# Performance work log

Measured on AMD Instinct MI355X. Metric: run time of the kernel, lower is better.

## Reference

```python
import jax, jax.numpy as jnp
import numpy as np

B, T, D = 8, 1, 4096          # batch, fresh tokens (single-token decode), d_model
H, HD, KV = 32, 128, 512      # n_heads, head_dim, mla_kv_lrank
PAST = 8191                   # cached compressed-KV length
SCALE = HD ** -0.5


def setup_inputs() -> dict:
    key = jax.random.key(0)
    ks = jax.random.split(key, 6)
    return {
        "x": jax.random.normal(ks[0], (B, T, D), dtype=jnp.float32),
        "past_c": jax.random.normal(ks[1], (B, PAST, KV), dtype=jnp.float32),
        # absorbed q*k_up projection: [H, D, KV]
        "absorbed_qk": jax.random.normal(ks[2], (H, D, KV), dtype=jnp.float32) * 0.02,
        # _compress_kv: Linear(D -> KV)
        "w_compress": jax.random.normal(ks[3], (D, KV), dtype=jnp.float32) * 0.02,
        # v_up: Linear(KV -> H*HD)
        "w_v": jax.random.normal(ks[4], (KV, H * HD), dtype=jnp.float32) * 0.02,
        # out_proj: Linear(H*HD -> D)
        "w_o": jax.random.normal(ks[5], (H * HD, D), dtype=jnp.float32) * 0.02,
    }


def reference(x, past_c, absorbed_qk, w_compress, w_v, w_o):
    b, t, d = x.shape
    # compress fresh tokens and extend the compressed KV cache
    c = x @ w_compress                                 # [B, T, KV]
    c_full = jnp.concatenate([past_c, c], axis=1)      # [B, total, KV]
    total = c_full.shape[1]

    # absorbed query projection: Q_abs = x @ absorbed_qk per head
    q_abs = jnp.einsum('btd,hdk->bhtk', x, absorbed_qk)        # [B, H, T, KV]
    # attention scores directly against compressed cache
    scores = jnp.einsum('bhtk,bsk->bhts', q_abs, c_full) * SCALE  # [B, H, T, total]

    # causal mask: query t (absolute pos total-T+t) sees kv pos p iff p <= total-T+t
    q_pos = jnp.arange(t)[:, None] + (total - t)       # [T, 1]
    kv_pos = jnp.arange(total)[None, :]                # [1, total]
    causal = q_pos >= kv_pos                           # [T, total]
    scores = jnp.where(causal[None, None], scores, -jnp.inf)
    attn = jax.nn.softmax(scores, axis=-1)             # [B, H, T, total]

    # up-project V from compressed cache
    v = (c_full @ w_v).reshape(b, total, H, HD)        # [B, total, H, HD]
    out = jnp.einsum('bhts,bshd->bthd', attn, v).reshape(b, t, H * HD)
    return out @ w_o                                   # [B, T, D]
```

## Files before the change

### kernel.cpp

```cpp
#include <hip/hip_runtime.h>
#include <stdint.h>

#define B_ 8
#define D_ 4096
#define H_ 32
#define HD_ 128
#define KV_ 512
#define PAST_ 8191
#define SCALE_ 0.08838834764831845f

#define OFF_QP   0u
#define OFF_CP   2097152u
#define OFF_QABS 2162688u
#define OFF_CNEW 2293760u
#define OFF_ML   2297856u
#define OFF_CTXP 2330624u
#define OFF_CTX2 10719232u

typedef float f32x4 __attribute__((ext_vector_type(4)));
typedef float f32x2 __attribute__((ext_vector_type(2)));
typedef short s16x8 __attribute__((ext_vector_type(8)));
typedef short s16x4 __attribute__((ext_vector_type(4)));

__device__ __forceinline__ unsigned short f2bf(float f) {
    unsigned u = __float_as_uint(f);
    u = (u + 0x7FFFu + ((u >> 16) & 1u)) >> 16;
    return (unsigned short)u;
}
__device__ __forceinline__ float bf2f(unsigned short s) {
    return __uint_as_float(((unsigned)s) << 16);
}

__global__ __launch_bounds__(128) void k_qabs(const float* __restrict__ x,
                                              const float* __restrict__ aqk,
                                              const float* __restrict__ wc,
                                              float* __restrict__ ws) {
    const int h = blockIdx.x;
    const int dc = blockIdx.y;
    const int t = threadIdx.x;
    alignas(16) __shared__ float x_lds[B_][256];
    for (int i = t; i < 512; i += 128) {
        const int b = i >> 6, g = i & 63;
        *(f32x4*)&x_lds[b][g * 4] = *(const f32x4*)(x + (size_t)b * D_ + dc * 256 + g * 4);
    }
    __syncthreads();
    const float* A = (h < H_) ? (aqk + (size_t)h * D_ * KV_) : wc;
    A += ((size_t)dc * 256) * KV_ + t * 4;

    f32x4 acc[B_];
#pragma unroll
    for (int b = 0; b < B_; ++b) acc[b] = (f32x4){0.f, 0.f, 0.f, 0.f};

#pragma unroll 2
    for (int dd = 0; dd < 256; dd += 4) {
        const f32x4 a0 = *(const f32x4*)(A + (size_t)(dd + 0) * KV_);
        const f32x4 a1 = *(const f32x4*)(A + (size_t)(dd + 1) * KV_);
        const f32x4 a2 = *(const f32x4*)(A + (size_t)(dd + 2) * KV_);
        const f32x4 a3 = *(const f32x4*)(A + (size_t)(dd + 3) * KV_);
#pragma unroll
        for (int b = 0; b < B_; ++b) {
            const f32x4 xq = *(const f32x4*)&x_lds[b][dd];
            acc[b] += xq.x * a0 + xq.y * a1 + xq.z * a2 + xq.w * a3;
        }
    }
#pragma unroll
    for (int b = 0; b < B_; ++b) {
        float* dst = (h < H_)
            ? (ws + OFF_QP + (size_t)dc * 131072u + (size_t)(b * H_ + h) * KV_ + t * 4)
            : (ws + OFF_CP + (size_t)dc * 4096u + (size_t)b * KV_ + t * 4);
        *(f32x4*)dst = acc[b];
    }
}

__global__ __launch_bounds__(256) void k_qred(float* __restrict__ ws) {
    const int bx = blockIdx.x;
    const int t = threadIdx.x;
    if (bx < 256) {
        const int b = bx >> 5, h = bx & 31;
        const size_t row = (size_t)(b * H_ + h) * KV_;
        f32x2 s = {0.f, 0.f};
#pragma unroll
        for (int p = 0; p < 16; ++p) {
            const f32x2 v = *(const f32x2*)(ws + OFF_QP + (size_t)p * 131072u + row + 2 * t);
            s[0] += v[0]; s[1] += v[1];
        }
        *(f32x2*)(ws + OFF_QABS + row + 2 * t) = s;
    } else {
        const int b = bx - 256;
        f32x2 s = {0.f, 0.f};
#pragma unroll
        for (int p = 0; p < 16; ++p) {
            const f32x2 v = *(const f32x2*)(ws + OFF_CP + (size_t)p * 4096u + (size_t)b * KV_ + 2 * t);
            s[0] += v[0]; s[1] += v[1];
        }
        *(f32x2*)(ws + OFF_CNEW + (size_t)b * KV_ + 2 * t) = s;
    }
}

__global__ __launch_bounds__(256, 2) void k_attn(const float* __restrict__ past_c,
                                                 float* __restrict__ ws) {
    const int bx = blockIdx.x;
    const int b = bx >> 6, sc = bx & 63;
    const int t = threadIdx.x;
    const int w = t >> 6, lane = t & 63, quad = lane >> 4, ln = lane & 15;
    const int ni = w & 1, kh = w >> 1;

    alignas(16) __shared__ unsigned short ch[16 * 520];
    alignas(16) __shared__ unsigned short cl[16 * 520];
    alignas(16) __shared__ unsigned short cT[512 * 20];
    alignas(16) __shared__ float Sp[2 * 16 * 33];
    alignas(16) __shared__ unsigned short P[32 * 20];
    __shared__ float alpha[32];

    s16x8 qh[8], ql[8];
    {
        const float* qp = ws + OFF_QABS + (size_t)(b * H_ + ni * 16 + ln) * KV_ + kh * 256 + quad * 8;
#pragma unroll
        for (int st = 0; st < 8; ++st) {
            const f32x4 v0 = *(const f32x4*)(qp + st * 32);
            const f32x4 v1 = *(const f32x4*)(qp + st * 32 + 4);
#pragma unroll
            for (int i = 0; i < 8; ++i) {
                const float xv = ((i < 4) ? v0[i] : v1[i - 4]) * SCALE_;
                const unsigned short hi = f2bf(xv);
                qh[st][i] = (short)hi;
                ql[st][i] = (short)f2bf(xv - bf2f(hi));
            }
        }
    }

    f32x4 cacc[16];
#pragma unroll
    for (int i = 0; i < 16; ++i) cacc[i] = (f32x4){0.f, 0.f, 0.f, 0.f};
    float m_run = -1e30f, l_run = 0.f;

    for (int sub = 0; sub < 8; ++sub) {
        const int s0 = sc * 128 + sub * 16;
        {
            const int r = t >> 4, m = t & 15;
            const int sg = s0 + r;
            const float* src = (sg == PAST_) ? (ws + OFF_CNEW + (size_t)b * KV_)
                                             : (past_c + ((size_t)b * PAST_ + sg) * KV_);
#pragma unroll
            for (int i = 0; i < 8; ++i) {
                const int k = m * 4 + i * 64;
                const f32x4 v = *(const f32x4*)(src + k);
                s16x4 hi4, lo4;
#pragma unroll
                for (int e = 0; e < 4; ++e) {
                    const unsigned short hh = f2bf(v[e]);
                    hi4[e] = (short)hh;
                    lo4[e] = (short)f2bf(v[e] - bf2f(hh));
                    const int kk = k + e;
                    cT[kk * 20 + (r ^ ((((kk) >> 4) & 3) << 2))] = hh;
                }
                *(s16x4*)&ch[r * 520 + k] = hi4;
                *(s16x4*)&cl[r * 520 + k] = lo4;
            }
        }
        __syncthreads();
        {
            f32x4 sacc = {0.f, 0.f, 0.f, 0.f};
#pragma unroll
            for (int st = 0; st < 8; ++st) {
                const int ko = kh * 256 + st * 32 + quad * 8;
                const s16x8 ah = *(const s16x8*)&ch[ln * 520 + ko];
                const s16x8 al = *(const s16x8*)&cl[ln * 520 + ko];
                sacc = __builtin_amdgcn_mfma_f32_16x16x32_bf16(ah, qh[st], sacc, 0, 0, 0);
                sacc = __builtin_amdgcn_mfma_f32_16x16x32_bf16(ah, ql[st], sacc, 0, 0, 0);
                sacc = __builtin_amdgcn_mfma_f32_16x16x32_bf16(al, qh[st], sacc, 0, 0, 0);
            }
#pragma unroll
            for (int r = 0; r < 4; ++r)
                Sp[kh * 528 + (quad * 4 + r) * 33 + ni * 16 + ln] = sacc[r];
        }
        __syncthreads();
        if (t < 32) {
            const int h = t;
            float sv[16];
            float msub = -1e30f;
#pragma unroll
            for (int s = 0; s < 16; ++s) {
                sv[s] = Sp[s * 33 + h] + Sp[528 + s * 33 + h];
                msub = fmaxf(msub, sv[s]);
            }
            const float m_new = fmaxf(m_run, msub);
            const float al_ = __expf(m_run - m_new);
            float lsum = 0.f;
#pragma unroll
            for (int s = 0; s < 16; s += 2) {
                const float p0 = __expf(sv[s] - m_new);
                const float p1 = __expf(sv[s + 1] - m_new);
                lsum += p0 + p1;
                const unsigned pk = (unsigned)f2bf(p0) | ((unsigned)f2bf(p1) << 16);
                *(unsigned*)&P[h * 20 + s] = pk;
            }
            l_run = l_run * al_ + lsum;
            m_run = m_new;
            alpha[h] = al_;
        }
        __syncthreads();
        {
            const float av = alpha[ni * 16 + ln];
            const s16x4 bp = *(const s16x4*)&P[(ni * 16 + ln) * 20 + quad * 4];
#pragma unroll
            for (int ti = 0; ti < 16; ++ti) {
                const int krow = (kh * 16 + ti) * 16 + ln;
                const int sg2 = (quad ^ ((krow >> 4) & 3)) << 2;
                const s16x4 ac = *(const s16x4*)&cT[krow * 20 + sg2];
                f32x4 cc = cacc[ti];
                cc[0] *= av; cc[1] *= av; cc[2] *= av; cc[3] *= av;
                cacc[ti] = __builtin_amdgcn_mfma_f32_16x16x16bf16_1k(ac, bp, cc, 0, 0, 0);
            }
        }
        __syncthreads();
    }
    {
        float* cp = ws + OFF_CTXP + ((size_t)(b * 64 + sc) * H_ + (ni * 16 + ln)) * KV_;
#pragma unroll
        for (int ti = 0; ti < 16; ++ti) {
            const int k0 = (kh * 16 + ti) * 16 + quad * 4;
            *(f32x4*)(cp + k0) = cacc[ti];
        }
    }
    if (t < 32) {
        float* mp = ws + OFF_ML + (size_t)(b * 64 + sc) * 64;
        mp[t] = m_run;
        mp[32 + t] = l_run;
    }
}

__global__ __launch_bounds__(256) void k_cv(const float* __restrict__ wv,
                                            float* __restrict__ ws) {
    const int b = blockIdx.x >> 5, h = blockIdx.x & 31;
    const int t = threadIdx.x;
    __shared__ float ml[64], ll[64], wgt[64];
    alignas(16) __shared__ float cx[512];
    alignas(16) __shared__ float red[8][128];
    if (t < 64) {
        const float* mp = ws + OFF_ML + (size_t)(b * 64 + t) * 64;
        ml[t] = mp[h];
        ll[t] = mp[32 + h];
    }
    __syncthreads();
    float M = -1e30f;
    for (int s = 0; s < 64; ++s) M = fmaxf(M, ml[s]);
    if (t < 64) wgt[t] = __expf(ml[t] - M);
    __syncthreads();
    float L = 0.f;
    for (int s = 0; s < 64; ++s) L += ll[s] * wgt[s];
    const float invL = 1.f / L;
    f32x2 acc = {0.f, 0.f};
    for (int s = 0; s < 64; ++s) {
        const float f = wgt[s];
        const f32x2 v = *(const f32x2*)(ws + OFF_CTXP + ((size_t)(b * 64 + s) * H_ + h) * KV_ + 2 * t);
        acc[0] += f * v[0];
        acc[1] += f * v[1];
    }
    *(f32x2*)&cx[2 * t] = (f32x2){acc[0] * invL, acc[1] * invL};
    __syncthreads();
    const int r = t >> 5, c = (t & 31) * 4;
    f32x4 a4 = {0.f, 0.f, 0.f, 0.f};
    for (int kb = 0; kb < 64; ++kb) {
        const int k = kb * 8 + r;
        const f32x4 w4 = *(const f32x4*)(wv + (size_t)k * (H_ * HD_) + h * HD_ + c);
        a4 += cx[k] * w4;
    }
    *(f32x4*)&red[r][c] = a4;
    __syncthreads();
    if (t < 128) {
        float s = 0.f;
#pragma unroll
        for (int rr = 0; rr < 8; ++rr) s += red[rr][t];
        ws[OFF_CTX2 + (size_t)b * D_ + h * HD_ + t] = s;
    }
}

__global__ __launch_bounds__(256) void k_out(const float* __restrict__ wo,
                                             const float* __restrict__ ws,
                                             float* __restrict__ out) {
    const int dc = blockIdx.x, jc = blockIdx.y;
    const int t = threadIdx.x;
    alignas(16) __shared__ float c2[B_][256];
#pragma unroll
    for (int i = 0; i < 8; ++i) {
        const int e = t + i * 256;
        const int bb = e >> 8, jj = e & 255;
        c2[bb][jj] = ws[OFF_CTX2 + (size_t)bb * D_ + jc * 256 + jj];
    }
    __syncthreads();
    const int d = dc * 256 + t;
    float acc[B_] = {};
    for (int j = 0; j < 256; j += 8) {
        float wreg[8];
#pragma unroll
        for (int u = 0; u < 8; ++u)
            wreg[u] = wo[(size_t)(jc * 256 + j + u) * D_ + d];
#pragma unroll
        for (int b = 0; b < B_; ++b) {
            const f32x4 c0 = *(const f32x4*)&c2[b][j];
            const f32x4 c1 = *(const f32x4*)&c2[b][j + 4];
            acc[b] += c0[0] * wreg[0] + c0[1] * wreg[1] + c0[2] * wreg[2] + c0[3] * wreg[3]
                    + c1[0] * wreg[4] + c1[1] * wreg[5] + c1[2] * wreg[6] + c1[3] * wreg[7];
        }
    }
#pragma unroll
    for (int b = 0; b < B_; ++b)
        atomicAdd(&out[b * D_ + d], acc[b]);
}

extern "C" void kernel_launch(void* const* d_in, const int* in_sizes, int n_in,
                              void* d_out, int out_size, void* d_ws, size_t ws_size,
                              hipStream_t stream) {
    const float* x      = (const float*)d_in[0];
    const float* past_c = (const float*)d_in[1];
    const float* aqk    = (const float*)d_in[2];
    const float* wc     = (const float*)d_in[3];
    const float* wv     = (const float*)d_in[4];
    const float* wo     = (const float*)d_in[5];
    float* out = (float*)d_out;
    float* ws  = (float*)d_ws;

    hipMemsetAsync(d_out, 0, (size_t)out_size * sizeof(float), stream);

    k_qabs<<<dim3(33, 16), 128, 0, stream>>>(x, aqk, wc, ws);
    k_qred<<<dim3(264), 256, 0, stream>>>(ws);
    k_attn<<<dim3(512), 256, 0, stream>>>(past_c, ws);
    k_cv<<<dim3(256), 256, 0, stream>>>(wv, ws);
    k_out<<<dim3(16, 16), 256, 0, stream>>>(wo, ws, out);
}
```

Baseline: 551.2 us.

## Split q_abs projection into finer D-chunks and widen reduction and cv kernels

The absorbed-query projection now splits D into 64 chunks of 64 rows instead of 16 chunks of 256, which quadruples the grid. Each thread loads 16 rows of weights ahead of the FMAs, and x is stored transposed in LDS so one vector read covers all batches. The reduction kernel and the context-combine/V-projection kernel go to 512 threads, each doing a two-way split with an LDS combine. This targets the 268 MB absorbed_qk read, which is bandwidth-bound and lacks parallelism, at the cost of four times the partial-sum traffic and a larger workspace.

```diff
diff --git a/kernel.cpp b/kernel.cpp
--- a/kernel.cpp
+++ b/kernel.cpp
@@ -10,12 +10,12 @@
 #define SCALE_ 0.08838834764831845f
 
 #define OFF_QP   0u
-#define OFF_CP   2097152u
-#define OFF_QABS 2162688u
-#define OFF_CNEW 2293760u
-#define OFF_ML   2297856u
-#define OFF_CTXP 2330624u
-#define OFF_CTX2 10719232u
+#define OFF_CP   8388608u
+#define OFF_QABS 8650752u
+#define OFF_CNEW 8781824u
+#define OFF_ML   8785920u
+#define OFF_CTXP 8818688u
+#define OFF_CTX2 17207296u
 
 typedef float f32x4 __attribute__((ext_vector_type(4)));
 typedef float f32x2 __attribute__((ext_vector_type(2)));
@@ -38,29 +38,38 @@
     const int h = blockIdx.x;
     const int dc = blockIdx.y;
     const int t = threadIdx.x;
-    alignas(16) __shared__ float x_lds[B_][256];
-    for (int i = t; i < 512; i += 128) {
-        const int b = i >> 6, g = i & 63;
-        *(f32x4*)&x_lds[b][g * 4] = *(const f32x4*)(x + (size_t)b * D_ + dc * 256 + g * 4);
-    }
-    __syncthreads();
-    const float* A = (h < H_) ? (aqk + (size_t)h * D_ * KV_) : wc;
-    A += ((size_t)dc * 256) * KV_ + t * 4;
+    alignas(16) __shared__ float xT[64][8];
+    {
+        const int b = t >> 4, g = t & 15;
+        const f32x4 v = *(const f32x4*)(x + (size_t)b * D_ + dc * 64 + g * 4);
+#pragma unroll
+        for (int e = 0; e < 4; ++e) xT[g * 4 + e][b] = v[e];
+    }
+    __syncthreads();
+    const float* A = ((h < H_) ? (aqk + (size_t)h * D_ * KV_) : wc)
+                   + ((size_t)dc * 64) * KV_ + t * 4;
 
     f32x4 acc[B_];
 #pragma unroll
     for (int b = 0; b < B_; ++b) acc[b] = (f32x4){0.f, 0.f, 0.f, 0.f};
 
-#pragma unroll 2
-    for (int dd = 0; dd < 256; dd += 4) {
-        const f32x4 a0 = *(const f32x4*)(A + (size_t)(dd + 0) * KV_);
-        const f32x4 a1 = *(const f32x4*)(A + (size_t)(dd + 1) * KV_);
-        const f32x4 a2 = *(const f32x4*)(A + (size_t)(dd + 2) * KV_);
-        const f32x4 a3 = *(const f32x4*)(A + (size_t)(dd + 3) * KV_);
-#pragma unroll
-        for (int b = 0; b < B_; ++b) {
-            const f32x4 xq = *(const f32x4*)&x_lds[b][dd];
-            acc[b] += xq.x * a0 + xq.y * a1 + xq.z * a2 + xq.w * a3;
+    for (int r0 = 0; r0 < 64; r0 += 16) {
+        f32x4 a[16];
+#pragma unroll
+        for (int u = 0; u < 16; ++u)
+            a[u] = *(const f32x4*)(A + (size_t)(r0 + u) * KV_);
+#pragma unroll
+        for (int u = 0; u < 16; ++u) {
+            const f32x4 xa = *(const f32x4*)&xT[r0 + u][0];
+            const f32x4 xb = *(const f32x4*)&xT[r0 + u][4];
+            acc[0] += xa[0] * a[u];
+            acc[1] += xa[1] * a[u];
+            acc[2] += xa[2] * a[u];
+            acc[3] += xa[3] * a[u];
+            acc[4] += xb[0] * a[u];
+            acc[5] += xb[1] * a[u];
+            acc[6] += xb[2] * a[u];
+            acc[7] += xb[3] * a[u];
         }
     }
 #pragma unroll
@@ -72,28 +81,37 @@
     }
 }
 
-__global__ __launch_bounds__(256) void k_qred(float* __restrict__ ws) {
+__global__ __launch_bounds__(512) void k_qred(float* __restrict__ ws) {
     const int bx = blockIdx.x;
     const int t = threadIdx.x;
+    const int pg = t >> 8, tt = t & 255;
+    alignas(16) __shared__ float part[2][512];
+
+    const float* src;
+    size_t stride;
+    float* dst;
     if (bx < 256) {
-        const int b = bx >> 5, h = bx & 31;
-        const size_t row = (size_t)(b * H_ + h) * KV_;
-        f32x2 s = {0.f, 0.f};
-#pragma unroll
-        for (int p = 0; p < 16; ++p) {
-            const f32x2 v = *(const f32x2*)(ws + OFF_QP + (size_t)p * 131072u + row + 2 * t);
-            s[0] += v[0]; s[1] += v[1];
-        }
-        *(f32x2*)(ws + OFF_QABS + row + 2 * t) = s;
+        src = ws + OFF_QP + (size_t)pg * 32u * 131072u + (size_t)bx * KV_ + 2 * tt;
+        stride = 131072u;
+        dst = ws + OFF_QABS + (size_t)bx * KV_;
     } else {
         const int b = bx - 256;
-        f32x2 s = {0.f, 0.f};
-#pragma unroll
-        for (int p = 0; p < 16; ++p) {
-            const f32x2 v = *(const f32x2*)(ws + OFF_CP + (size_t)p * 4096u + (size_t)b * KV_ + 2 * t);
-            s[0] += v[0]; s[1] += v[1];
-        }
-        *(f32x2*)(ws + OFF_CNEW + (size_t)b * KV_ + 2 * t) = s;
+        src = ws + OFF_CP + (size_t)pg * 32u * 4096u + (size_t)b * KV_ + 2 * tt;
+        stride = 4096u;
+        dst = ws + OFF_CNEW + (size_t)b * KV_;
+    }
+    f32x2 s = {0.f, 0.f};
+#pragma unroll 8
+    for (int p = 0; p < 32; ++p) {
+        const f32x2 v = *(const f32x2*)(src + (size_t)p * stride);
+        s[0] += v[0]; s[1] += v[1];
+    }
+    *(f32x2*)&part[pg][2 * tt] = s;
+    __syncthreads();
+    if (t < 256) {
+        const f32x2 p0 = *(const f32x2*)&part[0][2 * t];
+        const f32x2 p1 = *(const f32x2*)&part[1][2 * t];
+        *(f32x2*)(dst + 2 * t) = (f32x2){p0[0] + p1[0], p0[1] + p1[1]};
     }
 }
 
@@ -230,13 +248,14 @@
     }
 }
 
-__global__ __launch_bounds__(256) void k_cv(const float* __restrict__ wv,
+__global__ __launch_bounds__(512) void k_cv(const float* __restrict__ wv,
                                             float* __restrict__ ws) {
     const int b = blockIdx.x >> 5, h = blockIdx.x & 31;
     const int t = threadIdx.x;
     __shared__ float ml[64], ll[64], wgt[64];
     alignas(16) __shared__ float cx[512];
-    alignas(16) __shared__ float red[8][128];
+    alignas(16) __shared__ float cpart[2][512];
+    alignas(16) __shared__ float red[16][128];
     if (t < 64) {
         const float* mp = ws + OFF_ML + (size_t)(b * 64 + t) * 64;
         ml[t] = mp[h];
@@ -250,19 +269,28 @@
     float L = 0.f;
     for (int s = 0; s < 64; ++s) L += ll[s] * wgt[s];
     const float invL = 1.f / L;
+    const int half = t >> 8, tt = t & 255;
     f32x2 acc = {0.f, 0.f};
-    for (int s = 0; s < 64; ++s) {
+#pragma unroll 8
+    for (int s = half; s < 64; s += 2) {
         const float f = wgt[s];
-        const f32x2 v = *(const f32x2*)(ws + OFF_CTXP + ((size_t)(b * 64 + s) * H_ + h) * KV_ + 2 * t);
+        const f32x2 v = *(const f32x2*)(ws + OFF_CTXP + ((size_t)(b * 64 + s) * H_ + h) * KV_ + 2 * tt);
         acc[0] += f * v[0];
         acc[1] += f * v[1];
     }
-    *(f32x2*)&cx[2 * t] = (f32x2){acc[0] * invL, acc[1] * invL};
+    *(f32x2*)&cpart[half][2 * tt] = acc;
+    __syncthreads();
+    if (t < 256) {
+        const f32x2 p0 = *(const f32x2*)&cpart[0][2 * t];
+        const f32x2 p1 = *(const f32x2*)&cpart[1][2 * t];
+        *(f32x2*)&cx[2 * t] = (f32x2){(p0[0] + p1[0]) * invL, (p0[1] + p1[1]) * invL};
+    }
     __syncthreads();
     const int r = t >> 5, c = (t & 31) * 4;
     f32x4 a4 = {0.f, 0.f, 0.f, 0.f};
-    for (int kb = 0; kb < 64; ++kb) {
-        const int k = kb * 8 + r;
+#pragma unroll 4
+    for (int kb = 0; kb < 32; ++kb) {
+        const int k = kb * 16 + r;
         const f32x4 w4 = *(const f32x4*)(wv + (size_t)k * (H_ * HD_) + h * HD_ + c);
         a4 += cx[k] * w4;
     }
@@ -271,7 +299,7 @@
     if (t < 128) {
         float s = 0.f;
 #pragma unroll
-        for (int rr = 0; rr < 8; ++rr) s += red[rr][t];
+        for (int rr = 0; rr < 16; ++rr) s += red[rr][t];
         ws[OFF_CTX2 + (size_t)b * D_ + h * HD_ + t] = s;
     }
 }
@@ -323,9 +351,9 @@
 
     hipMemsetAsync(d_out, 0, (size_t)out_size * sizeof(float), stream);
 
-    k_qabs<<<dim3(33, 16), 128, 0, stream>>>(x, aqk, wc, ws);
-    k_qred<<<dim3(264), 256, 0, stream>>>(ws);
+    k_qabs<<<dim3(33, 64), 128, 0, stream>>>(x, aqk, wc, ws);
+    k_qred<<<dim3(264), 512, 0, stream>>>(ws);
     k_attn<<<dim3(512), 256, 0, stream>>>(past_c, ws);
-    k_cv<<<dim3(256), 256, 0, stream>>>(wv, ws);
+    k_cv<<<dim3(256), 512, 0, stream>>>(wv, ws);
     k_out<<<dim3(16, 16), 256, 0, stream>>>(wo, ws, out);
 }
```

Result: no change. 561.7 us (+1.9%).
